# Kernel tuning notes

Hardware: AMD Instinct MI355X
Metric: run time of the kernel (lower is better)

The kernel has to match this reference:

```python
import jax, jax.numpy as jnp
import numpy as np

M = 1024       # number of retained frequency bins (init kwarg m)
LMBDA = 0.1    # regularizer (init kwarg lmbda)


def _next_pow2(n):
    return 1 << int(np.ceil(np.log2(n)))


def _single_fv(ts, m):
    # ts: [b, L, d] real. Zero-pad time to next pow2, FFT along time, keep first m bins.
    b, L, d = ts.shape
    Lp = _next_pow2(L)
    x = jnp.pad(ts, ((0, 0), (0, Lp - L), (0, 0))).transpose(0, 2, 1)  # [b, d, Lp]
    Q = jnp.fft.fft(x.astype(jnp.complex64), axis=-1)                   # unnormalized FFT (matches legacy torch.fft)
    return Q[:, :, :m]                                                   # [b, d, m] complex


def setup_inputs() -> dict:
    key = jax.random.key(0)
    k1, k2, k3 = jax.random.split(key, 3)
    B, L, D = 16, 4096, 512
    max_len = 4096
    return {
        "ts_a": jax.random.normal(k1, (B, L, D), dtype=jnp.float32),
        "ts_b": jax.random.normal(k2, (B, L, D), dtype=jnp.float32),
        "offsets": jax.random.normal(k3, (B, 2 * max_len), dtype=jnp.float32),
    }


def reference(ts_a, ts_b, offsets):
    m, lmbda = M, LMBDA
    Qa = _single_fv(ts_a, m)            # [b, d, m]
    Qb = _single_fv(ts_b, m)
    max_len = offsets.shape[-1] // 2    # merge() re-derives max_len from offsets
    Lp2 = _next_pow2(max_len)

    def corr(Q, B_):
        # regularized circulant cross-correlation in the Fourier domain
        den = jnp.sum(Q.real * Q.real + Q.imag * Q.imag, axis=1, keepdims=True) + lmbda  # [b,1,m]
        S = jnp.sum(jnp.conj(Q) * B_, axis=1, keepdims=True) / den                       # [b,1,m]
        S = jnp.pad(S, ((0, 0), (0, 0), (0, Lp2 - m)))                                   # pad freq bins
        R = jnp.fft.ifft(S, axis=-1).real                                                # normalized IFFT (matches torch.ifft)
        return R[:, 0, :max_len]                                                          # [b, max_len]

    Rab = corr(Qa, Qb)
    Rba = corr(Qb, Qa)
    return jnp.concatenate([Rab[:, ::-1], Rba], axis=1)  # first half flipped, as in torch code
```

## Files before the change

kernel.cpp:

```cpp
#include <hip/hip_runtime.h>

#define NB 16
#define LT 4096
#define ND 512
#define MBINS 1024
#define LMBDA 0.1f
#define DLB 8
#define ZS 9
#define FWD_THREADS 1024

__device__ __forceinline__ float2 cmulf(float2 a, float2 b) {
    return make_float2(a.x * b.x - a.y * b.y, a.x * b.y + a.y * b.x);
}
__device__ __forceinline__ float2 caddf(float2 a, float2 b) { return make_float2(a.x + b.x, a.y + b.y); }
__device__ __forceinline__ float2 csubf(float2 a, float2 b) { return make_float2(a.x - b.x, a.y - b.y); }

__device__ __forceinline__ int rev4_10(int k) {
    unsigned r = __brev((unsigned)k) >> 22;
    return (int)(((r & 0x155u) << 1) | ((r >> 1) & 0x155u));
}
__device__ __forceinline__ int rev4_12(int t) {
    unsigned r = __brev((unsigned)t) >> 20;
    return (int)(((r & 0x555u) << 1) | ((r >> 1) & 0x555u));
}


__global__ __launch_bounds__(FWD_THREADS)
void cte_fwd_kernel(const float* __restrict__ A, const float* __restrict__ Bp,
                    float* __restrict__ ws) {
    __shared__ float2 z[1024 * ZS];
    __shared__ float2 tw[256];

    const int tid = threadIdx.x;
    const int logical = (blockIdx.x & 7) * (gridDim.x >> 3) + (blockIdx.x >> 3);
    const int bb    = logical >> 6;
    const int chunk = logical & 63;
    const int d0    = chunk * DLB;

    if (tid < 256) {
        float s, c;
        sincosf(-6.283185307179586f * (float)tid * (1.0f / 1024.0f), &s, &c);
        tw[tid] = make_float2(c, s);
    }

    const int dl = tid & (DLB - 1);
    const int g  = tid >> 3;
    const int dp  = tid & 3;
    const int t1l = tid >> 2;

    float2 X1[8], Z4[8];
#pragma unroll
    for (int j = 0; j < 8; ++j) {
        X1[j] = make_float2(0.f, 0.f);
        Z4[j] = make_float2(0.f, 0.f);
    }

    for (int t2 = 0; t2 < 4; ++t2) {
        __syncthreads();

        float2 A4[4], B4[4];
#pragma unroll
        for (int it = 0; it < 4; ++it) {
            size_t off = ((size_t)(bb * LT + 4 * (t1l + 256 * it) + t2)) * ND + d0 + 2 * dp;
            A4[it] = *(const float2*)(A + off);
            B4[it] = *(const float2*)(Bp + off);
        }
        {
            float2 w1 = tw[t1l & 255];
            float2 w2 = cmulf(w1, w1);
            float2 w3 = cmulf(w2, w1);
#pragma unroll
            for (int c = 0; c < 2; ++c) {
                float2 x0 = c ? make_float2(A4[0].y, B4[0].y) : make_float2(A4[0].x, B4[0].x);
                float2 x1 = c ? make_float2(A4[1].y, B4[1].y) : make_float2(A4[1].x, B4[1].x);
                float2 x2 = c ? make_float2(A4[2].y, B4[2].y) : make_float2(A4[2].x, B4[2].x);
                float2 x3 = c ? make_float2(A4[3].y, B4[3].y) : make_float2(A4[3].x, B4[3].x);
                float2 t0  = caddf(x0, x2), t1v = csubf(x0, x2);
                float2 t2v = caddf(x1, x3), t3  = csubf(x1, x3);
                float2 y0 = caddf(t0, t2v);
                float2 y2 = cmulf(csubf(t0, t2v), w2);
                float2 y1 = cmulf(make_float2(t1v.x + t3.y, t1v.y - t3.x), w1);
                float2 y3 = cmulf(make_float2(t1v.x - t3.y, t1v.y + t3.x), w3);
                int col = 2 * dp + c;
                z[(t1l)       * ZS + col] = y0;
                z[(t1l + 256) * ZS + col] = y1;
                z[(t1l + 512) * ZS + col] = y2;
                z[(t1l + 768) * ZS + col] = y3;
            }
        }
        __syncthreads();

#pragma unroll
        for (int st = 1; st < 5; ++st) {
            const int lgm  = 8 - 2 * st;
            const int m    = 1 << lgm;
            const int step = 256 >> lgm;
#pragma unroll
            for (int r = 0; r < 2; ++r) {
                int u   = r * FWD_THREADS + tid;
                int dli = u & (DLB - 1);
                int bf  = u >> 3;
                int j   = bf & (m - 1);
                int i0  = ((bf >> lgm) << (lgm + 2)) + j;
                float2 a0 = z[(i0)         * ZS + dli];
                float2 a1 = z[(i0 + m)     * ZS + dli];
                float2 a2 = z[(i0 + 2 * m) * ZS + dli];
                float2 a3 = z[(i0 + 3 * m) * ZS + dli];
                float2 t0  = caddf(a0, a2), t1v = csubf(a0, a2);
                float2 t2v = caddf(a1, a3), t3  = csubf(a1, a3);
                float2 y0 = caddf(t0, t2v);
                float2 y2 = csubf(t0, t2v);
                float2 y1 = make_float2(t1v.x + t3.y, t1v.y - t3.x);
                float2 y3 = make_float2(t1v.x - t3.y, t1v.y + t3.x);
                if (m > 1) {
                    float2 w1 = tw[j * step];
                    float2 w2 = cmulf(w1, w1);
                    float2 w3 = cmulf(w2, w1);
                    y1 = cmulf(y1, w1);
                    y2 = cmulf(y2, w2);
                    y3 = cmulf(y3, w3);
                }
                z[(i0)         * ZS + dli] = y0;
                z[(i0 + m)     * ZS + dli] = y1;
                z[(i0 + 2 * m) * ZS + dli] = y2;
                z[(i0 + 3 * m) * ZS + dli] = y3;
            }
            __syncthreads();
        }

        float2 w, wstep;
        {
            float s, c;
            sincosf(-1.5339807878856412e-03f * (float)(t2 * g), &s, &c);
            w = make_float2(c, s);
            sincosf(-1.9634954084936207e-01f * (float)t2, &s, &c);
            wstep = make_float2(c, s);
        }
#pragma unroll
        for (int j = 0; j < 8; ++j) {
            int k   = g + 128 * j;
            int rk  = rev4_10(k);
            int k2  = (1024 - k) & 1023;
            int rk2 = rev4_10(k2);
            float2 Ya = z[rk * ZS + dl];
            float2 Yb = z[rk2 * ZS + dl];
            X1[j].x += w.x * Ya.x - w.y * Ya.y;
            X1[j].y += w.x * Ya.y + w.y * Ya.x;
            Z4[j].x += w.x * Yb.x + w.y * Yb.y;
            Z4[j].y += w.x * Yb.y - w.y * Yb.x;
            w = cmulf(w, wstep);
        }
    }

#pragma unroll
    for (int j = 0; j < 8; ++j) {
        int k = g + 128 * j;
        float Ar = 0.5f * (X1[j].x + Z4[j].x);
        float Ai = 0.5f * (X1[j].y - Z4[j].y);
        float Br = 0.5f * (X1[j].y + Z4[j].y);
        float Bi = 0.5f * (Z4[j].x - X1[j].x);
        float da = Ar * Ar + Ai * Ai;
        float db = Br * Br + Bi * Bi;
        float cr = Ar * Br + Ai * Bi;
        float ci = Ar * Bi - Ai * Br;
        for (int msk = 1; msk < DLB; msk <<= 1) {
            da += __shfl_xor(da, msk);
            db += __shfl_xor(db, msk);
            cr += __shfl_xor(cr, msk);
            ci += __shfl_xor(ci, msk);
        }
        if (dl == 0) {
            atomicAdd(&ws[0 * NB * MBINS + bb * MBINS + k], da);
            atomicAdd(&ws[1 * NB * MBINS + bb * MBINS + k], db);
            atomicAdd(&ws[2 * NB * MBINS + bb * MBINS + k], cr);
            atomicAdd(&ws[3 * NB * MBINS + bb * MBINS + k], ci);
        }
    }
}

__global__ __launch_bounds__(512)
void cte_inv_kernel(const float* __restrict__ ws, float* __restrict__ out) {
    __shared__ float2 zz[4096];
    __shared__ float2 tw[1024];
    const int tid = threadIdx.x;
    const int bb  = blockIdx.x >> 1;
    const int dir = blockIdx.x & 1;

    for (int i = tid; i < 1024; i += 512) {
        float s, c;
        sincosf(6.283185307179586f * (float)i * (1.0f / 4096.0f), &s, &c);
        tw[i] = make_float2(c, s);
    }
    for (int i = tid; i < 4096; i += 512) {
        float2 v = make_float2(0.f, 0.f);
        if (i < MBINS) {
            float den = ws[(dir ? 1 : 0) * NB * MBINS + bb * MBINS + i] + LMBDA;
            float cr  = ws[2 * NB * MBINS + bb * MBINS + i];
            float ci  = ws[3 * NB * MBINS + bb * MBINS + i];
            if (dir) ci = -ci;
            v = make_float2(cr / den, ci / den);
        }
        zz[i] = v;
    }
    __syncthreads();

#pragma unroll
    for (int st = 0; st < 6; ++st) {
        const int lgm  = 10 - 2 * st;
        const int m    = 1 << lgm;
        const int step = 1024 >> lgm;
#pragma unroll
        for (int r = 0; r < 2; ++r) {
            int bf = r * 512 + tid;
            int j  = bf & (m - 1);
            int i0 = ((bf >> lgm) << (lgm + 2)) + j;
            float2 a0 = zz[i0], a1 = zz[i0 + m], a2 = zz[i0 + 2 * m], a3 = zz[i0 + 3 * m];
            float2 t0  = caddf(a0, a2), t1v = csubf(a0, a2);
            float2 t2v = caddf(a1, a3), t3  = csubf(a1, a3);
            float2 y0 = caddf(t0, t2v);
            float2 y2 = csubf(t0, t2v);
            float2 y1 = make_float2(t1v.x - t3.y, t1v.y + t3.x);
            float2 y3 = make_float2(t1v.x + t3.y, t1v.y - t3.x);
            if (m > 1) {
                float2 w1 = tw[j * step];
                float2 w2 = cmulf(w1, w1);
                float2 w3 = cmulf(w2, w1);
                y1 = cmulf(y1, w1);
                y2 = cmulf(y2, w2);
                y3 = cmulf(y3, w3);
            }
            zz[i0] = y0; zz[i0 + m] = y1; zz[i0 + 2 * m] = y2; zz[i0 + 3 * m] = y3;
        }
        __syncthreads();
    }

    const float scale = 1.0f / 4096.0f;
    for (int t = tid; t < 4096; t += 512) {
        int rt = rev4_12(t);
        float val = zz[rt].x * scale;
        int col = (dir == 0) ? (4095 - t) : (4096 + t);
        out[(size_t)bb * 8192 + col] = val;
    }
}

extern "C" void kernel_launch(void* const* d_in, const int* in_sizes, int n_in,
                              void* d_out, int out_size, void* d_ws, size_t ws_size,
                              hipStream_t stream) {
    const float* a = (const float*)d_in[0];
    const float* b = (const float*)d_in[1];
    float* out = (float*)d_out;
    float* ws  = (float*)d_ws;

    hipMemsetAsync(d_ws, 0, 4 * NB * MBINS * sizeof(float), stream);
    cte_fwd_kernel<<<dim3(NB * (ND / DLB)), dim3(FWD_THREADS), 0, stream>>>(a, b, ws);
    cte_inv_kernel<<<dim3(NB * 2), dim3(512), 0, stream>>>(ws, out);
}
```

Measured before the change: 214.9 us.

## Fuse last radix-4 stage with final twiddle accumulation and drop LDS padding

The forward kernel now runs three shared-memory radix-4 stages instead of four. The last stage is fused into the register accumulation of the t2 decimation, and the conjugate-mirror term (Z4) is derived algebraically through a fixed ±1/±i rotation instead of a second bit-reversed LDS read. LDS padding (ZS=9) is removed in favour of a dense stride-8 layout. Mirror bins are exchanged through one extra shared-memory round-trip before the reduction. This cuts LDS traffic and barriers per t2 iteration, at the risk of more bank conflicts from the unpadded layout and extra complex multiplies.

```diff
diff --git a/kernel.cpp b/kernel.cpp
--- a/kernel.cpp
+++ b/kernel.cpp
@@ -6,7 +6,6 @@
 #define MBINS 1024
 #define LMBDA 0.1f
 #define DLB 8
-#define ZS 9
 #define FWD_THREADS 1024
 
 __device__ __forceinline__ float2 cmulf(float2 a, float2 b) {
@@ -15,9 +14,8 @@
 __device__ __forceinline__ float2 caddf(float2 a, float2 b) { return make_float2(a.x + b.x, a.y + b.y); }
 __device__ __forceinline__ float2 csubf(float2 a, float2 b) { return make_float2(a.x - b.x, a.y - b.y); }
 
-__device__ __forceinline__ int rev4_10(int k) {
-    unsigned r = __brev((unsigned)k) >> 22;
-    return (int)(((r & 0x155u) << 1) | ((r >> 1) & 0x155u));
+__device__ __forceinline__ int rev4_8(int k) {
+    return ((k & 3) << 6) | ((k & 12) << 2) | ((k >> 2) & 12) | ((k >> 6) & 3);
 }
 __device__ __forceinline__ int rev4_12(int t) {
     unsigned r = __brev((unsigned)t) >> 20;
@@ -28,7 +26,7 @@
 __global__ __launch_bounds__(FWD_THREADS)
 void cte_fwd_kernel(const float* __restrict__ A, const float* __restrict__ Bp,
                     float* __restrict__ ws) {
-    __shared__ float2 z[1024 * ZS];
+    __shared__ float2 z[8192];
     __shared__ float2 tw[256];
 
     const int tid = threadIdx.x;
@@ -43,16 +41,17 @@
         tw[tid] = make_float2(c, s);
     }
 
-    const int dl = tid & (DLB - 1);
-    const int g  = tid >> 3;
+    const int dl  = tid & 7;
+    const int bfa = tid >> 3;
+    const int rb0 = rev4_8(bfa);
     const int dp  = tid & 3;
     const int t1l = tid >> 2;
 
-    float2 X1[8], Z4[8];
-#pragma unroll
-    for (int j = 0; j < 8; ++j) {
-        X1[j] = make_float2(0.f, 0.f);
-        Z4[j] = make_float2(0.f, 0.f);
+    float2 X1[8], G[8];
+#pragma unroll
+    for (int i = 0; i < 8; ++i) {
+        X1[i] = make_float2(0.f, 0.f);
+        G[i]  = make_float2(0.f, 0.f);
     }
 
     for (int t2 = 0; t2 < 4; ++t2) {
@@ -66,7 +65,7 @@
             B4[it] = *(const float2*)(Bp + off);
         }
         {
-            float2 w1 = tw[t1l & 255];
+            float2 w1 = tw[t1l];
             float2 w2 = cmulf(w1, w1);
             float2 w3 = cmulf(w2, w1);
 #pragma unroll
@@ -81,99 +80,124 @@
                 float2 y2 = cmulf(csubf(t0, t2v), w2);
                 float2 y1 = cmulf(make_float2(t1v.x + t3.y, t1v.y - t3.x), w1);
                 float2 y3 = cmulf(make_float2(t1v.x - t3.y, t1v.y + t3.x), w3);
-                int col = 2 * dp + c;
-                z[(t1l)       * ZS + col] = y0;
-                z[(t1l + 256) * ZS + col] = y1;
-                z[(t1l + 512) * ZS + col] = y2;
-                z[(t1l + 768) * ZS + col] = y3;
+                int ix = (t1l << 3) + 2 * dp + c;
+                z[ix]            = y0;
+                z[ix + 256 * 8]  = y1;
+                z[ix + 512 * 8]  = y2;
+                z[ix + 768 * 8]  = y3;
             }
         }
         __syncthreads();
 
 #pragma unroll
-        for (int st = 1; st < 5; ++st) {
-            const int lgm  = 8 - 2 * st;
+        for (int st = 0; st < 3; ++st) {
+            const int lgm  = 6 - 2 * st;
             const int m    = 1 << lgm;
             const int step = 256 >> lgm;
 #pragma unroll
-            for (int r = 0; r < 2; ++r) {
-                int u   = r * FWD_THREADS + tid;
-                int dli = u & (DLB - 1);
+            for (int r2 = 0; r2 < 2; ++r2) {
+                int u   = r2 * FWD_THREADS + tid;
+                int dli = u & 7;
                 int bf  = u >> 3;
                 int j   = bf & (m - 1);
                 int i0  = ((bf >> lgm) << (lgm + 2)) + j;
-                float2 a0 = z[(i0)         * ZS + dli];
-                float2 a1 = z[(i0 + m)     * ZS + dli];
-                float2 a2 = z[(i0 + 2 * m) * ZS + dli];
-                float2 a3 = z[(i0 + 3 * m) * ZS + dli];
+                int ix  = (i0 << 3) + dli;
+                float2 a0 = z[ix];
+                float2 a1 = z[ix + 8 * m];
+                float2 a2 = z[ix + 16 * m];
+                float2 a3 = z[ix + 24 * m];
                 float2 t0  = caddf(a0, a2), t1v = csubf(a0, a2);
                 float2 t2v = caddf(a1, a3), t3  = csubf(a1, a3);
-                float2 y0 = caddf(t0, t2v);
-                float2 y2 = csubf(t0, t2v);
-                float2 y1 = make_float2(t1v.x + t3.y, t1v.y - t3.x);
-                float2 y3 = make_float2(t1v.x - t3.y, t1v.y + t3.x);
-                if (m > 1) {
-                    float2 w1 = tw[j * step];
-                    float2 w2 = cmulf(w1, w1);
-                    float2 w3 = cmulf(w2, w1);
-                    y1 = cmulf(y1, w1);
-                    y2 = cmulf(y2, w2);
-                    y3 = cmulf(y3, w3);
-                }
-                z[(i0)         * ZS + dli] = y0;
-                z[(i0 + m)     * ZS + dli] = y1;
-                z[(i0 + 2 * m) * ZS + dli] = y2;
-                z[(i0 + 3 * m) * ZS + dli] = y3;
+                float2 w1 = tw[j * step];
+                float2 w2 = cmulf(w1, w1);
+                float2 w3 = cmulf(w2, w1);
+                z[ix]          = caddf(t0, t2v);
+                z[ix + 8 * m]  = cmulf(make_float2(t1v.x + t3.y, t1v.y - t3.x), w1);
+                z[ix + 16 * m] = cmulf(csubf(t0, t2v), w2);
+                z[ix + 24 * m] = cmulf(make_float2(t1v.x - t3.y, t1v.y + t3.x), w3);
             }
             __syncthreads();
         }
 
-        float2 w, wstep;
+        float2 wr, w16, w2s;
         {
             float s, c;
-            sincosf(-1.5339807878856412e-03f * (float)(t2 * g), &s, &c);
-            w = make_float2(c, s);
-            sincosf(-1.9634954084936207e-01f * (float)t2, &s, &c);
-            wstep = make_float2(c, s);
-        }
-#pragma unroll
-        for (int j = 0; j < 8; ++j) {
-            int k   = g + 128 * j;
-            int rk  = rev4_10(k);
-            int k2  = (1024 - k) & 1023;
-            int rk2 = rev4_10(k2);
-            float2 Ya = z[rk * ZS + dl];
-            float2 Yb = z[rk2 * ZS + dl];
-            X1[j].x += w.x * Ya.x - w.y * Ya.y;
-            X1[j].y += w.x * Ya.y + w.y * Ya.x;
-            Z4[j].x += w.x * Yb.x + w.y * Yb.y;
-            Z4[j].y += w.x * Yb.y - w.y * Yb.x;
-            w = cmulf(w, wstep);
-        }
-    }
-
-#pragma unroll
-    for (int j = 0; j < 8; ++j) {
-        int k = g + 128 * j;
-        float Ar = 0.5f * (X1[j].x + Z4[j].x);
-        float Ai = 0.5f * (X1[j].y - Z4[j].y);
-        float Br = 0.5f * (X1[j].y + Z4[j].y);
-        float Bi = 0.5f * (Z4[j].x - X1[j].x);
-        float da = Ar * Ar + Ai * Ai;
-        float db = Br * Br + Bi * Bi;
-        float cr = Ar * Br + Ai * Bi;
-        float ci = Ar * Bi - Ai * Br;
-        for (int msk = 1; msk < DLB; msk <<= 1) {
-            da += __shfl_xor(da, msk);
-            db += __shfl_xor(db, msk);
-            cr += __shfl_xor(cr, msk);
-            ci += __shfl_xor(ci, msk);
-        }
-        if (dl == 0) {
-            atomicAdd(&ws[0 * NB * MBINS + bb * MBINS + k], da);
-            atomicAdd(&ws[1 * NB * MBINS + bb * MBINS + k], db);
-            atomicAdd(&ws[2 * NB * MBINS + bb * MBINS + k], cr);
-            atomicAdd(&ws[3 * NB * MBINS + bb * MBINS + k], ci);
+            sincosf(-1.5339807878856412e-03f * (float)(t2 * rb0), &s, &c);
+            wr = make_float2(c, s);
+            sincosf(-3.9269908169872414e-01f * (float)t2, &s, &c);
+            w16 = make_float2(c, s);
+            sincosf(-3.0679615757712823e-03f * (float)t2, &s, &c);
+            w2s = make_float2(c, s);
+        }
+        const float mix = (t2 & 1) ? 0.f : ((t2 & 2) ? -1.f : 1.f);
+        const float miy = (t2 & 1) ? ((t2 & 2) ? -1.f : 1.f) : 0.f;
+
+#pragma unroll
+        for (int bfi = 0; bfi < 2; ++bfi) {
+            int ix = ((bfa + 128 * bfi) << 5) + dl;
+            float2 a0 = z[ix];
+            float2 a1 = z[ix + 8];
+            float2 a2 = z[ix + 16];
+            float2 a3 = z[ix + 24];
+            float2 t0  = caddf(a0, a2), t1v = csubf(a0, a2);
+            float2 t2v = caddf(a1, a3), t3  = csubf(a1, a3);
+            float2 yy[4];
+            yy[0] = caddf(t0, t2v);
+            yy[1] = make_float2(t1v.x + t3.y, t1v.y - t3.x);
+            yy[2] = csubf(t0, t2v);
+            yy[3] = make_float2(t1v.x - t3.y, t1v.y + t3.x);
+            float2 wb = bfi ? cmulf(wr, w2s) : wr;
+#pragma unroll
+            for (int q = 0; q < 4; ++q) {
+                float2 p = cmulf(wb, yy[q]);
+                int i = (bfi << 2) + q;
+                X1[i] = caddf(X1[i], p);
+                G[i].x += mix * p.x - miy * p.y;
+                G[i].y += mix * p.y + miy * p.x;
+                wb = cmulf(wb, w16);
+            }
+        }
+    }
+
+    __syncthreads();
+#pragma unroll
+    for (int bfi = 0; bfi < 2; ++bfi) {
+#pragma unroll
+        for (int q = 0; q < 4; ++q) {
+            int mbin = 256 * q + rb0 + 2 * bfi;
+            z[(mbin << 3) + dl] = X1[(bfi << 2) + q];
+        }
+    }
+    __syncthreads();
+#pragma unroll
+    for (int bfi = 0; bfi < 2; ++bfi) {
+#pragma unroll
+        for (int q = 0; q < 4; ++q) {
+            int i    = (bfi << 2) + q;
+            int mbin = 256 * q + rb0 + 2 * bfi;
+            int k0   = (1024 - mbin) & 1023;
+            float2 P  = z[(k0 << 3) + dl];
+            float2 Xm = (mbin == 0) ? P : G[i];
+            float Ar = 0.5f * (P.x + Xm.x);
+            float Ai = 0.5f * (P.y - Xm.y);
+            float Br = 0.5f * (P.y + Xm.y);
+            float Bi = 0.5f * (Xm.x - P.x);
+            float da = Ar * Ar + Ai * Ai;
+            float db = Br * Br + Bi * Bi;
+            float cr = Ar * Br + Ai * Bi;
+            float ci = Ar * Bi - Ai * Br;
+            for (int msk = 1; msk < DLB; msk <<= 1) {
+                da += __shfl_xor(da, msk);
+                db += __shfl_xor(db, msk);
+                cr += __shfl_xor(cr, msk);
+                ci += __shfl_xor(ci, msk);
+            }
+            if (dl == 0) {
+                atomicAdd(&ws[0 * NB * MBINS + bb * MBINS + k0], da);
+                atomicAdd(&ws[1 * NB * MBINS + bb * MBINS + k0], db);
+                atomicAdd(&ws[2 * NB * MBINS + bb * MBINS + k0], cr);
+                atomicAdd(&ws[3 * NB * MBINS + bb * MBINS + k0], ci);
+            }
         }
     }
 }
```

Result: slower. 530.7 us (+147.0%).
